# Performance work log

Hardware: AMD Instinct MI355X
Metric: run time of the kernel (lower is better)

## Reference

```python
import jax, jax.numpy as jnp
import numpy as np

B, L, D, H = 8, 512, 1024, 16
HD = D // H  # head dim = 64
SCALE = 1.0  # scale=False in __init__


def _rel_sinusoid(seq_len, dim):
    # RelativeSinusoidalPositionalEmbedding lookup for relative positions
    # arange(-L/2, L/2) (even L), sinusoid of the raw relative position.
    half = dim // 2
    inv = jnp.exp(jnp.arange(half, dtype=jnp.float32) * (-(np.log(10000.0) / (half - 1))))
    r = jnp.arange(-(seq_len // 2), seq_len // 2, dtype=jnp.float32)  # (L,)
    ang = r[:, None] * inv[None, :]  # (L, half)
    return jnp.concatenate([jnp.sin(ang), jnp.cos(ang)], axis=1)  # (L, dim)


def setup_inputs() -> dict:
    key = jax.random.key(0)
    ks = jax.random.split(key, 8)
    s = 0.02
    x = jax.random.normal(ks[0], (B, L, D), jnp.float32)
    mask = jax.random.randint(ks[1], (B, L), 0, 2).astype(jnp.int64)
    mask = mask.at[:, 0].set(1)  # ensure at least one valid key per row
    qmask = jax.random.randint(ks[2], (B, L), 0, 2).astype(jnp.int64)
    w_qkv = jax.random.normal(ks[3], (D, 3 * D), jnp.float32) * s
    w_qkpos = jax.random.normal(ks[4], (HD, 2 * D), jnp.float32) * s
    w_fc = jax.random.normal(ks[5], (D, D), jnp.float32) * s
    b_fc = jnp.zeros((D,), jnp.float32)
    shift = jnp.abs(jax.random.normal(ks[6], (1,), jnp.float32)) + 0.001
    bias = -jnp.abs(jax.random.normal(ks[7], (1,), jnp.float32))
    return dict(x=x, mask=mask, qmask=qmask, w_qkv=w_qkv, w_qkpos=w_qkpos,
                w_fc=w_fc, b_fc=b_fc, shift=shift, bias=bias)


def reference(x, mask, qmask, w_qkv, w_qkpos, w_fc, b_fc, shift, bias):
    # trans_type='self', use_Gaussian=True, dropout in eval mode (identity)
    b, l, d = x.shape
    qkv = x @ w_qkv  # (B, L, 3D)
    q, k, v = jnp.split(qkv, 3, axis=-1)
    q = q.reshape(b, l, H, HD).transpose(0, 2, 1, 3)  # (B,H,L,hd)
    k = k.reshape(b, l, H, HD).transpose(0, 2, 1, 3)
    v = v.reshape(b, l, H, HD).transpose(0, 2, 1, 3)

    pe = _rel_sinusoid(l, HD)               # (L, hd)
    y = pe @ w_qkpos                        # (L, 2D)
    q_p, k_p = jnp.split(y, 2, axis=-1)     # (L, D) each
    q_p = q_p.reshape(l, H, HD).transpose(1, 0, 2)  # (H, L, hd)
    k_p = k_p.reshape(l, H, HD).transpose(1, 0, 2)  # (H, L, hd)

    attn = jnp.einsum('bhid,bhjd->bhij', q, k) + jnp.einsum('hid,hjd->hij', q_p, k_p)[None]

    # speaker-identity masking: zero out cross-speaker scores (trans_type='self')
    qsame = qmask[:, :, None] == qmask[:, None, :]  # (B, L, L)
    attn = jnp.where(qsame[:, None], attn, 0.0)
    attn = attn / SCALE

    # key padding mask -> -inf
    attn = jnp.where(mask[:, None, None, :] == 0, -jnp.inf, attn)

    # Gaussian distance bias: -(shift * (i-j)^2 + bias)
    idx = jnp.arange(l, dtype=jnp.float32)
    sqd = (idx[:, None] - idx[None, :]) ** 2  # (L, L)
    attn = attn + (-(shift[0] * sqd + bias[0]))[None, None]

    attn = jax.nn.softmax(attn, axis=-1)
    out = jnp.einsum('bhij,bhjd->bhid', attn, v)  # (B,H,L,hd)
    out = out.transpose(0, 2, 1, 3).reshape(b, l, d)
    return out @ w_fc + b_fc
```

## Files before the change

### kernel.cpp

```cpp
#include <hip/hip_runtime.h>
#include <hip/hip_bf16.h>

#define BB 8
#define LL 512
#define DD 1024
#define HH 16
#define HD 64
#define LOG2E 1.4426950408889634f

typedef __attribute__((ext_vector_type(8))) unsigned short u16x8;
typedef __attribute__((ext_vector_type(4))) unsigned short u16x4;
typedef __attribute__((ext_vector_type(8))) __bf16 bf16x8;
typedef __attribute__((ext_vector_type(4))) float f32x4;
typedef __attribute__((ext_vector_type(16))) float f32x16;

#define DEV __device__ __forceinline__

DEV unsigned short f2bf(float f) {
    return __builtin_bit_cast(unsigned short, (__bf16)f);
}
DEV f32x4 mfma16(u16x8 a, u16x8 b, f32x4 c) {
    return __builtin_amdgcn_mfma_f32_16x16x32_bf16(
        __builtin_bit_cast(bf16x8, a), __builtin_bit_cast(bf16x8, b), c, 0, 0, 0);
}
DEV f32x16 mfma32(u16x8 a, u16x8 b, f32x16 c) {
    return __builtin_amdgcn_mfma_f32_32x32x16_bf16(
        __builtin_bit_cast(bf16x8, a), __builtin_bit_cast(bf16x8, b), c, 0, 0, 0);
}
typedef __attribute__((address_space(1))) void gv_t;
typedef __attribute__((address_space(3))) void lv_t;
DEV void gload16(const void* g, void* l) {
    __builtin_amdgcn_global_load_lds((gv_t*)g, (lv_t*)l, 16, 0, 0);
}


__global__ __launch_bounds__(256) void prep(
    const float* __restrict__ x, unsigned short* __restrict__ xb,
    const float* __restrict__ w_qkv, unsigned short* __restrict__ wqt,
    const float* __restrict__ w_fc, unsigned short* __restrict__ wft,
    const float* __restrict__ w_qkp, unsigned short* __restrict__ qpx,
    unsigned short* __restrict__ kpx) {
    __shared__ __align__(16) char lds[24576];
    int blk = blockIdx.x;
    int t = threadIdx.x;
    if (blk < 4096) {
        int i = blk * 256 + t;
        f32x4 v = *(const f32x4*)(x + i * 4);
        u16x4 o;
        o[0] = f2bf(v[0]); o[1] = f2bf(v[1]);
        o[2] = f2bf(v[2]); o[3] = f2bf(v[3]);
        *(u16x4*)(xb + i * 4) = o;
    } else if (blk < 7168) {
        int r = blk - 4096;
        int c0 = (r % 96) * 32, r0 = (r / 96) * 32;
        auto tile = (unsigned short(*)[33])lds;
        int tx = t & 31, ty = t >> 5;
#pragma unroll
        for (int i = 0; i < 32; i += 8)
            tile[ty + i][tx] = f2bf(w_qkv[(r0 + ty + i) * 3072 + c0 + tx]);
        __syncthreads();
#pragma unroll
        for (int i = 0; i < 32; i += 8)
            wqt[(c0 + ty + i) * 1024 + r0 + tx] = tile[tx][ty + i];
    } else if (blk < 8192) {
        int r = blk - 7168;
        int c0 = (r % 32) * 32, r0 = (r / 32) * 32;
        auto tile = (unsigned short(*)[33])lds;
        int tx = t & 31, ty = t >> 5;
#pragma unroll
        for (int i = 0; i < 32; i += 8)
            tile[ty + i][tx] = f2bf(w_fc[(r0 + ty + i) * 1024 + c0 + tx]);
        __syncthreads();
#pragma unroll
        for (int i = 0; i < 32; i += 8)
            wft[(c0 + ty + i) * 1024 + r0 + tx] = tile[tx][ty + i];
    } else {
        int r = blk - 8192;
        int c0 = (r % 64) * 32, i0 = (r / 64) * 64;
        auto peS = (float(*)[64])lds;
        auto wS = (float(*)[32])(lds + 16384);
#pragma unroll
        for (int j = 0; j < 16; ++j) {
            int o = t + j * 256;
            int ri = o >> 6, d = o & 63, dd = d & 31;
            float inv = expf((float)dd * -0.2971077539347156f);
            float ang = (float)(i0 + ri - 256) * inv;
            peS[ri][d] = (d < 32) ? sinf(ang) : cosf(ang);
        }
#pragma unroll
        for (int j = 0; j < 8; ++j) {
            int o = t + j * 256;
            wS[o >> 5][o & 31] = w_qkp[(o >> 5) * 2048 + c0 + (o & 31)];
        }
        __syncthreads();
#pragma unroll
        for (int j = 0; j < 8; ++j) {
            int o = t + j * 256;
            int row = o >> 5, col = o & 31;
            float acc = 0.0f;
#pragma unroll
            for (int k = 0; k < 64; ++k) acc += peS[row][k] * wS[k][col];
            int c = c0 + col, i = i0 + row;
            int qt = i >> 5, lq = i & 31;
            int cc = (c < 1024) ? c : (c - 1024);
            int h = cc >> 6, kk = cc & 63;
            int ks = kk >> 4, h2 = (kk >> 3) & 1, jj = kk & 7;
            unsigned idx = ((unsigned)(h * 4096 + qt * 256 + ks * 64 +
                            h2 * 32 + lq) << 3) + jj;
            if (c < 1024) qpx[idx] = f2bf(acc * LOG2E);
            else          kpx[idx] = f2bf(acc);
        }
    }
}

template <int MODE>
__global__ __launch_bounds__(512) void gemm_bt(
    const unsigned short* __restrict__ A, const unsigned short* __restrict__ Bt,
    int M, int N, int K, int NBX, unsigned short* __restrict__ o0,
    unsigned short* __restrict__ o1, unsigned short* __restrict__ o2,
    float* __restrict__ fout, const float* __restrict__ bias) {
    __shared__ __align__(16) unsigned short As[3][128 * 32];
    __shared__ __align__(16) unsigned short Bs[3][128 * 32];
    int g = blockIdx.x;
    int swz = (g & 7) * (gridDim.x >> 3) + (g >> 3);
    int bx = swz % NBX, by = swz / NBX;
    int m0 = by * 128, n0 = bx * 128;
    int t = threadIdx.x;
    int w = t >> 6, l = t & 63, lg = l >> 4, lc = l & 15;
    int rh = w >> 2, cq = w & 3;

    f32x4 acc[4][2] = {};

    int sr = t >> 2;
    int sc = (t & 3) ^ ((t >> 3) & 3);
    const unsigned short* Ab = A + (m0 + sr) * K + sc * 8;
    const unsigned short* Bb = Bt + (n0 + sr) * K + sc * 8;
    int rsw = (lc >> 1) & 3;

    auto stage = [&](int buf, int k0) {
        gload16(Ab + k0, &As[buf][w * 512]);
        gload16(Bb + k0, &Bs[buf][w * 512]);
    };

    stage(0, 0);
    stage(1, 32);
    stage(2, 64);
    int cur = 0;
    for (int k0 = 0; k0 < K; k0 += 32) {
        int rem = (K - k0) >> 5;
        if (rem > 2)
            asm volatile("s_waitcnt vmcnt(4)" ::: "memory");
        else if (rem == 2)
            asm volatile("s_waitcnt vmcnt(2)" ::: "memory");
        else
            asm volatile("s_waitcnt vmcnt(0)" ::: "memory");
        __builtin_amdgcn_sched_barrier(0);
        __builtin_amdgcn_s_barrier();
        __builtin_amdgcn_sched_barrier(0);
        u16x8 af[4], bf[2];
#pragma unroll
        for (int mm = 0; mm < 4; ++mm)
            af[mm] = *(const u16x8*)&As[cur][(rh * 64 + mm * 16 + lc) * 32 +
                                             ((lg ^ rsw) << 3)];
#pragma unroll
        for (int nn = 0; nn < 2; ++nn)
            bf[nn] = *(const u16x8*)&Bs[cur][(cq * 32 + nn * 16 + lc) * 32 +
                                             ((lg ^ rsw) << 3)];
        asm volatile("s_waitcnt lgkmcnt(0)" ::: "memory");
        __builtin_amdgcn_sched_barrier(0);
        __builtin_amdgcn_s_barrier();
        __builtin_amdgcn_sched_barrier(0);
        if (k0 + 96 < K) stage(cur, k0 + 96);
#pragma unroll
        for (int mm = 0; mm < 4; ++mm)
#pragma unroll
            for (int nn = 0; nn < 2; ++nn)
                acc[mm][nn] = mfma16(af[mm], bf[nn], acc[mm][nn]);
        cur = (cur == 2) ? 0 : cur + 1;
    }

#pragma unroll
    for (int mm = 0; mm < 4; ++mm)
#pragma unroll
        for (int nn = 0; nn < 2; ++nn)
#pragma unroll
            for (int r = 0; r < 4; ++r) {
                int row = m0 + rh * 64 + mm * 16 + lg * 4 + r;
                int col = n0 + cq * 32 + nn * 16 + lc;
                float v = acc[mm][nn][r];
                if (MODE == 0) {
                    int bb = row >> 9, i = row & 511;
                    int which = col >> 10, dd = col & 1023;
                    int hh = dd >> 6, hd = dd & 63;
                    int bh2 = bb * HH + hh;
                    int tl = i >> 5, io = i & 31;
                    if (which == 2) {
                        int h2 = (io >> 2) & 1, ps = (io >> 4) & 1;
                        int j = (io & 3) | (((io >> 3) & 1) << 2);
                        int dblk = hd >> 5, lq = hd & 31;
                        unsigned idx = ((unsigned)(bh2 * 4096 + tl * 256 +
                                        (dblk * 2 + ps) * 64 + h2 * 32 + lq)
                                        << 3) + j;
                        o2[idx] = f2bf(v);
                    } else {
                        int ks = hd >> 4, h2 = (hd >> 3) & 1, j = hd & 7;
                        unsigned idx = ((unsigned)(bh2 * 4096 + tl * 256 +
                                        ks * 64 + h2 * 32 + io) << 3) + j;
                        if (which == 0) o0[idx] = f2bf(v * LOG2E);
                        else            o1[idx] = f2bf(v);
                    }
                } else {
                    fout[row * N + col] = v + bias[col];
                }
            }
}

__global__ __launch_bounds__(128, 1) void attn_k(
    const unsigned short* __restrict__ Qx, const unsigned short* __restrict__ Kx,
    const unsigned short* __restrict__ Vx, const unsigned short* __restrict__ QPx,
    const unsigned short* __restrict__ KPx, const int* __restrict__ mask,
    const int* __restrict__ qmask, const float* __restrict__ shp,
    unsigned short* __restrict__ out) {
    __shared__ float mbuf[2][64];
    __shared__ float lsbuf[2][64];
    __shared__ float obuf[2][64][33];

    int g = blockIdx.x;
    int bid = ((g & 7) << 7) + (g >> 3);
    int b = bid >> 7, h = (bid >> 3) & 15, qp = bid & 7;
    int t = threadIdx.x, kh = t >> 6, l = t & 63;
    int lq = l & 31, hi = l >> 5;
    int c0 = qp * 2;
    int qA = c0 * 32 + lq, qB = qA + 32;
    int bh = b * HH + h;

    const unsigned short* qbA  = Qx  + (((unsigned)(bh * 4096 + c0 * 256)) << 3) + (l << 3);
    const unsigned short* qpbA = QPx + (((unsigned)(h  * 4096 + c0 * 256)) << 3) + (l << 3);
    u16x8 qfA[4], pfA[4], qfB[4], pfB[4];
#pragma unroll
    for (int ks = 0; ks < 4; ++ks) {
        qfA[ks] = *(const u16x8*)(qbA + ks * 512);
        pfA[ks] = *(const u16x8*)(qpbA + ks * 512);
        qfB[ks] = *(const u16x8*)(qbA + 2048 + ks * 512);
        pfB[ks] = *(const u16x8*)(qpbA + 2048 + ks * 512);
    }

    unsigned long long km[4], qm[4];
#pragma unroll
    for (int t8 = 0; t8 < 4; ++t8) {
        int base = b * LL + (kh * 4 + t8) * 64 + l;
        km[t8] = __ballot(mask[base] != 0);
        qm[t8] = __ballot(qmask[base] != 0);
    }
    int qiA = (qmask[b * LL + qA] != 0) ? 1 : 0;
    int qiB = (qmask[b * LL + qB] != 0) ? 1 : 0;

    const float M0 = -1.0e30f, NEGF = -3.0e38f, THR = 8.0f;
    float negs = -(*shp) * LOG2E;
    float mA = M0, lsA = 0.0f, mB = M0, lsB = 0.0f;
    f32x16 oA0 = {}, oA1 = {}, oB0 = {}, oB1 = {};
    float fqA = (float)(qA - 4 * hi);
    float fqB = (float)(qB - 4 * hi);

#pragma unroll
    for (int tt = 0; tt < 8; ++tt) {
        int ttg = kh * 8 + tt;
        const unsigned short* kb  = Kx  + (((unsigned)(bh * 4096 + ttg * 256)) << 3) + (l << 3);
        const unsigned short* kpb = KPx + (((unsigned)(h  * 4096 + ttg * 256)) << 3) + (l << 3);
        const unsigned short* vb  = Vx  + (((unsigned)(bh * 4096 + ttg * 256)) << 3) + (l << 3);
        u16x8 kf[4], kpf[4], vf[4];
#pragma unroll
        for (int ks = 0; ks < 4; ++ks) {
            kf[ks]  = *(const u16x8*)(kb + ks * 512);
            kpf[ks] = *(const u16x8*)(kpb + ks * 512);
            vf[ks]  = *(const u16x8*)(vb + ks * 512);
        }
        f32x16 sA = {}, sB = {};
#pragma unroll
        for (int ks = 0; ks < 4; ++ks) {
            sA = mfma32(kf[ks], qfA[ks], sA);
            sB = mfma32(kf[ks], qfB[ks], sB);
        }
#pragma unroll
        for (int ks = 0; ks < 4; ++ks) {
            sA = mfma32(kpf[ks], pfA[ks], sA);
            sB = mfma32(kpf[ks], pfB[ks], sB);
        }

        unsigned kwn = ((unsigned)(km[tt >> 1] >> ((tt & 1) * 32))) >> (hi * 4);
        unsigned qwn = ((unsigned)(qm[tt >> 1] >> ((tt & 1) * 32))) >> (hi * 4);
        float btA = fqA - 32.0f * (float)ttg;
        float btB = fqB - 32.0f * (float)ttg;

        {
            float p[16];
#pragma unroll
            for (int r = 0; r < 16; ++r) {
                const int off = (r & 3) + 8 * (r >> 2);
                float v = sA[r];
                v = (((qwn >> off) & 1u) == (unsigned)qiA) ? v : 0.0f;
                float dr = btA - (float)off;
                v = __builtin_fmaf(negs * dr, dr, v);
                v = ((kwn >> off) & 1u) ? v : NEGF;
                p[r] = v;
            }
            float a0 = fmaxf(fmaxf(p[0], p[1]), fmaxf(p[2], p[3]));
            float a1 = fmaxf(fmaxf(p[4], p[5]), fmaxf(p[6], p[7]));
            float a2 = fmaxf(fmaxf(p[8], p[9]), fmaxf(p[10], p[11]));
            float a3 = fmaxf(fmaxf(p[12], p[13]), fmaxf(p[14], p[15]));
            float pmax = fmaxf(fmaxf(a0, a1), fmaxf(a2, a3));
            pmax = fmaxf(pmax, __shfl_xor(pmax, 32));
            if (!__all(pmax <= mA + THR)) {
                float mn = fmaxf(mA, pmax);
                float sc = __builtin_amdgcn_exp2f(mA - mn);
#pragma unroll
                for (int r = 0; r < 16; ++r) { oA0[r] *= sc; oA1[r] *= sc; }
                lsA *= sc;
                mA = mn;
            }
#pragma unroll
            for (int r = 0; r < 16; ++r) p[r] = __builtin_amdgcn_exp2f(p[r] - mA);
            lsA += (((p[0] + p[1]) + (p[2] + p[3])) + ((p[4] + p[5]) + (p[6] + p[7]))) +
                   (((p[8] + p[9]) + (p[10] + p[11])) +
                    ((p[12] + p[13]) + (p[14] + p[15])));
            u16x8 pf0, pf1;
#pragma unroll
            for (int j = 0; j < 8; ++j) { pf0[j] = f2bf(p[j]); pf1[j] = f2bf(p[8 + j]); }
            oA0 = mfma32(vf[0], pf0, oA0);
            oA0 = mfma32(vf[1], pf1, oA0);
            oA1 = mfma32(vf[2], pf0, oA1);
            oA1 = mfma32(vf[3], pf1, oA1);
        }
        {
            float p[16];
#pragma unroll
            for (int r = 0; r < 16; ++r) {
                const int off = (r & 3) + 8 * (r >> 2);
                float v = sB[r];
                v = (((qwn >> off) & 1u) == (unsigned)qiB) ? v : 0.0f;
                float dr = btB - (float)off;
                v = __builtin_fmaf(negs * dr, dr, v);
                v = ((kwn >> off) & 1u) ? v : NEGF;
                p[r] = v;
            }
            float a0 = fmaxf(fmaxf(p[0], p[1]), fmaxf(p[2], p[3]));
            float a1 = fmaxf(fmaxf(p[4], p[5]), fmaxf(p[6], p[7]));
            float a2 = fmaxf(fmaxf(p[8], p[9]), fmaxf(p[10], p[11]));
            float a3 = fmaxf(fmaxf(p[12], p[13]), fmaxf(p[14], p[15]));
            float pmax = fmaxf(fmaxf(a0, a1), fmaxf(a2, a3));
            pmax = fmaxf(pmax, __shfl_xor(pmax, 32));
            if (!__all(pmax <= mB + THR)) {
                float mn = fmaxf(mB, pmax);
                float sc = __builtin_amdgcn_exp2f(mB - mn);
#pragma unroll
                for (int r = 0; r < 16; ++r) { oB0[r] *= sc; oB1[r] *= sc; }
                lsB *= sc;
                mB = mn;
            }
#pragma unroll
            for (int r = 0; r < 16; ++r) p[r] = __builtin_amdgcn_exp2f(p[r] - mB);
            lsB += (((p[0] + p[1]) + (p[2] + p[3])) + ((p[4] + p[5]) + (p[6] + p[7]))) +
                   (((p[8] + p[9]) + (p[10] + p[11])) +
                    ((p[12] + p[13]) + (p[14] + p[15])));
            u16x8 pf0, pf1;
#pragma unroll
            for (int j = 0; j < 8; ++j) { pf0[j] = f2bf(p[j]); pf1[j] = f2bf(p[8 + j]); }
            oB0 = mfma32(vf[0], pf0, oB0);
            oB0 = mfma32(vf[1], pf1, oB0);
            oB1 = mfma32(vf[2], pf0, oB1);
            oB1 = mfma32(vf[3], pf1, oB1);
        }
    }

    if (kh == 1) {
        mbuf[0][l] = mA;  lsbuf[0][l] = lsA;
        mbuf[1][l] = mB;  lsbuf[1][l] = lsB;
#pragma unroll
        for (int r = 0; r < 16; ++r) {
            obuf[0][l][r] = oA0[r];
            obuf[0][l][16 + r] = oA1[r];
            obuf[1][l][r] = oB0[r];
            obuf[1][l][16 + r] = oB1[r];
        }
    }
    __syncthreads();
    if (kh == 0) {
        {
            float m1 = mbuf[0][l], ls1 = lsbuf[0][l];
            float mm = fmaxf(mA, m1);
            float sc0 = __builtin_amdgcn_exp2f(mA - mm);
            float sc1 = __builtin_amdgcn_exp2f(m1 - mm);
            float lsm = lsA * sc0 + ls1 * sc1;
            float rs = lsm + __shfl_xor(lsm, 32);
            float rinv = __builtin_amdgcn_rcpf(rs);
            unsigned short* ob = out + ((long)(b * LL + qA)) * DD + h * HD + hi * 4;
#pragma unroll
            for (int rg = 0; rg < 4; ++rg) {
                u16x4 pk0, pk1;
#pragma unroll
                for (int rr = 0; rr < 4; ++rr) {
                    int i = rg * 4 + rr;
                    float v0 = __builtin_fmaf(oA0[i], sc0, obuf[0][l][i] * sc1);
                    float v1 = __builtin_fmaf(oA1[i], sc0, obuf[0][l][16 + i] * sc1);
                    pk0[rr] = f2bf(v0 * rinv);
                    pk1[rr] = f2bf(v1 * rinv);
                }
                *(u16x4*)(ob + rg * 8) = pk0;
                *(u16x4*)(ob + 32 + rg * 8) = pk1;
            }
        }
        {
            float m1 = mbuf[1][l], ls1 = lsbuf[1][l];
            float mm = fmaxf(mB, m1);
            float sc0 = __builtin_amdgcn_exp2f(mB - mm);
            float sc1 = __builtin_amdgcn_exp2f(m1 - mm);
            float lsm = lsB * sc0 + ls1 * sc1;
            float rs = lsm + __shfl_xor(lsm, 32);
            float rinv = __builtin_amdgcn_rcpf(rs);
            unsigned short* ob = out + ((long)(b * LL + qB)) * DD + h * HD + hi * 4;
#pragma unroll
            for (int rg = 0; rg < 4; ++rg) {
                u16x4 pk0, pk1;
#pragma unroll
                for (int rr = 0; rr < 4; ++rr) {
                    int i = rg * 4 + rr;
                    float v0 = __builtin_fmaf(oB0[i], sc0, obuf[1][l][i] * sc1);
                    float v1 = __builtin_fmaf(oB1[i], sc0, obuf[1][l][16 + i] * sc1);
                    pk0[rr] = f2bf(v0 * rinv);
                    pk1[rr] = f2bf(v1 * rinv);
                }
                *(u16x4*)(ob + rg * 8) = pk0;
                *(u16x4*)(ob + 32 + rg * 8) = pk1;
            }
        }
    }
}

extern "C" void kernel_launch(void* const* d_in, const int* in_sizes, int n_in,
                              void* d_out, int out_size, void* d_ws,
                              size_t ws_size, hipStream_t stream) {
    const float* x     = (const float*)d_in[0];
    const int*   mask  = (const int*)d_in[1];
    const int*   qmask = (const int*)d_in[2];
    const float* w_qkv = (const float*)d_in[3];
    const float* w_qkp = (const float*)d_in[4];
    const float* w_fc  = (const float*)d_in[5];
    const float* b_fc  = (const float*)d_in[6];
    const float* shift = (const float*)d_in[7];

    char* ws = (char*)d_ws;
    unsigned short* xb   = (unsigned short*)(ws);
    unsigned short* qb   = (unsigned short*)(ws + 8388608);
    unsigned short* kb   = (unsigned short*)(ws + 16777216);
    unsigned short* vtb  = (unsigned short*)(ws + 25165824);
    unsigned short* qp   = (unsigned short*)(ws + 33554432);
    unsigned short* kp   = (unsigned short*)(ws + 34603008);
    unsigned short* wqt  = (unsigned short*)(ws + 35651584);
    unsigned short* wft  = (unsigned short*)(ws + 41943040);
    unsigned short* aout = (unsigned short*)(ws + 44040192);

    prep<<<8704, 256, 0, stream>>>(x, xb, w_qkv, wqt, w_fc, wft, w_qkp, qp, kp);
    gemm_bt<0><<<768, 512, 0, stream>>>(xb, wqt, 4096, 3072, 1024, 24, qb, kb,
                                        vtb, nullptr, nullptr);
    attn_k<<<1024, 128, 0, stream>>>(qb, kb, vtb, qp, kp, mask, qmask, shift,
                                     aout);
    gemm_bt<1><<<256, 512, 0, stream>>>(aout, wft, 4096, 1024, 1024, 8, nullptr,
                                        nullptr, nullptr, (float*)d_out, b_fc);
}
```

Before: 132.0 us.

## Replace QKV GEMM with 256x256-tile ping-pong pipelined kernel

The QKV projection GEMM moves from 128x128 tiles with a 3-stage LDS ring to 256x256 tiles (192 blocks) that split each K-tile into halves and double-buffer them. Global loads are interleaved with the MFMA phases, guarded by explicit vmcnt waits, barriers and s_setprio. The larger tiles raise arithmetic intensity and reuse per block, and the schedule aims to hide load latency. The cost is far fewer blocks (192 over the CU count), heavy register pressure from 32 accumulators, and more barriers per K step. The FC GEMM is split into its own specialised kernel.

```diff
diff --git a/kernel.cpp b/kernel.cpp
--- a/kernel.cpp
+++ b/kernel.cpp
@@ -113,12 +113,142 @@
     }
 }
 
-template <int MODE>
-__global__ __launch_bounds__(512) void gemm_bt(
+__global__ __launch_bounds__(512, 2) void gemm8p(
     const unsigned short* __restrict__ A, const unsigned short* __restrict__ Bt,
-    int M, int N, int K, int NBX, unsigned short* __restrict__ o0,
-    unsigned short* __restrict__ o1, unsigned short* __restrict__ o2,
-    float* __restrict__ fout, const float* __restrict__ bias) {
+    unsigned short* __restrict__ o0, unsigned short* __restrict__ o1,
+    unsigned short* __restrict__ o2) {
+    __shared__ __align__(16) unsigned short As[2][2][8192];
+    __shared__ __align__(16) unsigned short Bs[2][2][8192];
+    const int K = 1024;
+    int g = blockIdx.x;
+    int swz = (g & 7) * 24 + (g >> 3);
+    int bx = swz % 12, by = swz / 12;
+    int m0 = by * 256, n0 = bx * 256;
+    int t = threadIdx.x;
+    int w = t >> 6, l = t & 63, lg = (l >> 4) & 3, lc = l & 15;
+    int wr = w >> 2, wcn = w & 3;
+    int rsw = lc & 7;
+
+    const unsigned short* Abase =
+        A + (m0 + w * 8 + (l >> 3)) * K + (((l & 7) ^ ((l >> 3) & 7)) << 3);
+    const unsigned short* Bbase =
+        Bt + (n0 + w * 8 + (l >> 3)) * K + (((l & 7) ^ ((l >> 3) & 7)) << 3);
+
+    auto stA = [&](int db, int half, int tile) {
+        gload16(Abase + (half * 128) * K + tile * 64, &As[db][half][w * 512]);
+        gload16(Abase + (half * 128 + 64) * K + tile * 64,
+                &As[db][half][4096 + w * 512]);
+    };
+    auto stB = [&](int db, int half, int tile) {
+        gload16(Bbase + (half * 128) * K + tile * 64, &Bs[db][half][w * 512]);
+        gload16(Bbase + (half * 128 + 64) * K + tile * 64,
+                &Bs[db][half][4096 + w * 512]);
+    };
+
+    f32x4 acc[8][4] = {};
+    u16x8 af[8], bf[2];
+
+    stA(0, 0, 0); stA(0, 1, 0); stB(0, 0, 0); stB(0, 1, 0); stA(1, 0, 1);
+    asm volatile("s_waitcnt vmcnt(2)" ::: "memory");
+    __builtin_amdgcn_s_barrier();
+
+#pragma unroll
+    for (int i = 0; i < 8; ++i) {
+#pragma unroll
+        for (int half = 0; half < 2; ++half) {
+            const int db = half;
+            const int tile = 2 * i + half;
+            (void)tile;
+#pragma unroll
+            for (int pp = 0; pp < 4; ++pp) {
+                const int ks = pp >> 1;
+                const int nh = pp & 1;
+                if (nh == 0) {
+#pragma unroll
+                    for (int mf = 0; mf < 8; ++mf)
+                        af[mf] = *(const u16x8*)&As[db][wr]
+                            [(mf * 16 + lc) * 64 + (((ks * 4 + lg) ^ rsw) << 3)];
+                }
+#pragma unroll
+                for (int nf = 0; nf < 2; ++nf)
+                    bf[nf] = *(const u16x8*)&Bs[db][wcn >> 1]
+                        [((wcn & 1) * 64 + (nh * 2 + nf) * 16 + lc) * 64 +
+                         (((ks * 4 + lg) ^ rsw) << 3)];
+                if (half == 0) {
+                    if (pp == 0) stA(1, 1, 2 * i + 1);
+                    else if (pp == 1) stB(1, 0, 2 * i + 1);
+                    else if (pp == 2) stB(1, 1, 2 * i + 1);
+                    else if (i < 7) stA(0, 0, 2 * i + 2);
+                } else {
+                    if (i < 7) {
+                        if (pp == 0) stA(0, 1, 2 * i + 2);
+                        else if (pp == 1) stB(0, 0, 2 * i + 2);
+                        else if (pp == 2) stB(0, 1, 2 * i + 2);
+                        else stA(1, 0, 2 * i + 3);
+                    }
+                }
+                if (pp == 3) {
+                    if (half == 0) {
+                        if (i < 7)
+                            asm volatile("s_waitcnt vmcnt(2)" ::: "memory");
+                        else
+                            asm volatile("s_waitcnt vmcnt(0)" ::: "memory");
+                    } else if (i < 7) {
+                        asm volatile("s_waitcnt vmcnt(2)" ::: "memory");
+                    }
+                }
+                __builtin_amdgcn_s_barrier();
+                asm volatile("s_waitcnt lgkmcnt(0)" ::: "memory");
+                __builtin_amdgcn_sched_barrier(0);
+                __builtin_amdgcn_s_setprio(1);
+#pragma unroll
+                for (int mf = 0; mf < 8; ++mf)
+#pragma unroll
+                    for (int nf = 0; nf < 2; ++nf)
+                        acc[mf][nh * 2 + nf] =
+                            mfma16(af[mf], bf[nf], acc[mf][nh * 2 + nf]);
+                __builtin_amdgcn_s_setprio(0);
+                __builtin_amdgcn_s_barrier();
+            }
+        }
+    }
+
+#pragma unroll
+    for (int mf = 0; mf < 8; ++mf)
+#pragma unroll
+        for (int nf = 0; nf < 4; ++nf)
+#pragma unroll
+            for (int r = 0; r < 4; ++r) {
+                int row = m0 + wr * 128 + mf * 16 + lg * 4 + r;
+                int col = n0 + wcn * 64 + nf * 16 + lc;
+                float v = acc[mf][nf][r];
+                int bb = row >> 9, i = row & 511;
+                int which = col >> 10, dd = col & 1023;
+                int hh = dd >> 6, hd = dd & 63;
+                int bh2 = bb * HH + hh;
+                int tl = i >> 5, io = i & 31;
+                if (which == 2) {
+                    int h2 = (io >> 2) & 1, ps = (io >> 4) & 1;
+                    int j = (io & 3) | (((io >> 3) & 1) << 2);
+                    int dblk = hd >> 5, lq = hd & 31;
+                    unsigned idx = ((unsigned)(bh2 * 4096 + tl * 256 +
+                                    (dblk * 2 + ps) * 64 + h2 * 32 + lq)
+                                    << 3) + j;
+                    o2[idx] = f2bf(v);
+                } else {
+                    int ks = hd >> 4, h2 = (hd >> 3) & 1, j = hd & 7;
+                    unsigned idx = ((unsigned)(bh2 * 4096 + tl * 256 +
+                                    ks * 64 + h2 * 32 + io) << 3) + j;
+                    if (which == 0) o0[idx] = f2bf(v * LOG2E);
+                    else            o1[idx] = f2bf(v);
+                }
+            }
+}
+
+__global__ __launch_bounds__(512) void gemm_fc(
+    const unsigned short* __restrict__ A, const unsigned short* __restrict__ Bt,
+    int M, int N, int K, int NBX, float* __restrict__ fout,
+    const float* __restrict__ bias) {
     __shared__ __align__(16) unsigned short As[3][128 * 32];
     __shared__ __align__(16) unsigned short Bs[3][128 * 32];
     int g = blockIdx.x;
@@ -187,31 +317,7 @@
             for (int r = 0; r < 4; ++r) {
                 int row = m0 + rh * 64 + mm * 16 + lg * 4 + r;
                 int col = n0 + cq * 32 + nn * 16 + lc;
-                float v = acc[mm][nn][r];
-                if (MODE == 0) {
-                    int bb = row >> 9, i = row & 511;
-                    int which = col >> 10, dd = col & 1023;
-                    int hh = dd >> 6, hd = dd & 63;
-                    int bh2 = bb * HH + hh;
-                    int tl = i >> 5, io = i & 31;
-                    if (which == 2) {
-                        int h2 = (io >> 2) & 1, ps = (io >> 4) & 1;
-                        int j = (io & 3) | (((io >> 3) & 1) << 2);
-                        int dblk = hd >> 5, lq = hd & 31;
-                        unsigned idx = ((unsigned)(bh2 * 4096 + tl * 256 +
-                                        (dblk * 2 + ps) * 64 + h2 * 32 + lq)
-                                        << 3) + j;
-                        o2[idx] = f2bf(v);
-                    } else {
-                        int ks = hd >> 4, h2 = (hd >> 3) & 1, j = hd & 7;
-                        unsigned idx = ((unsigned)(bh2 * 4096 + tl * 256 +
-                                        ks * 64 + h2 * 32 + io) << 3) + j;
-                        if (which == 0) o0[idx] = f2bf(v * LOG2E);
-                        else            o1[idx] = f2bf(v);
-                    }
-                } else {
-                    fout[row * N + col] = v + bias[col];
-                }
+                fout[row * N + col] = acc[mm][nn][r] + bias[col];
             }
 }
 
@@ -460,10 +566,9 @@
     unsigned short* aout = (unsigned short*)(ws + 44040192);
 
     prep<<<8704, 256, 0, stream>>>(x, xb, w_qkv, wqt, w_fc, wft, w_qkp, qp, kp);
-    gemm_bt<0><<<768, 512, 0, stream>>>(xb, wqt, 4096, 3072, 1024, 24, qb, kb,
-                                        vtb, nullptr, nullptr);
+    gemm8p<<<192, 512, 0, stream>>>(xb, wqt, qb, kb, vtb);
     attn_k<<<1024, 128, 0, stream>>>(qb, kb, vtb, qp, kp, mask, qmask, shift,
                                      aout);
-    gemm_bt<1><<<256, 512, 0, stream>>>(aout, wft, 4096, 1024, 1024, 8, nullptr,
-                                        nullptr, nullptr, (float*)d_out, b_fc);
-}
+    gemm_fc<<<256, 512, 0, stream>>>(aout, wft, 4096, 1024, 1024, 8,
+                                     (float*)d_out, b_fc);
+}
```

Result: slower. 141.0 us (+6.8%).
